# Kernel optimization log

Hardware: AMD Instinct MI355X
Metric: run time of the kernel (lower is better)

## Reference

```python
import jax, jax.numpy as jnp
import numpy as np

EPS = 1e-4
B, T = 8192, 100
SEQ = T + 1          # 101: history + appended target token
D_EMB = 36           # 2*4 + 2*4 + 2*6 + 2*4
D_MODEL = 2 * D_EMB  # 72
NUM_TASKS = 10


def pos_table(periods, freqs):
    # PositionExpansion buffer: [periods+1, 2*freqs]
    i = jnp.arange(periods + 1, dtype=jnp.float32)[:, None]
    j = jnp.arange(freqs, dtype=jnp.float32)[None, :]
    ang = (np.pi / periods) * (2.0 ** j) * (i - 1.0)
    return jnp.concatenate([jnp.sin(ang), jnp.cos(ang)], axis=1)


def robust_scale(h, eps):
    # h: [B, T] float. Vectorized version of the per-sample RobustScaler loop.
    mask = h != 0
    cnt = mask.sum(1, keepdims=True).astype(h.dtype)              # [B,1]
    safe = jnp.maximum(cnt, 1.0)
    mean = jnp.where(mask, h, 0.0).sum(1, keepdims=True) / safe
    var = jnp.where(mask, (h - mean) ** 2, 0.0).sum(1, keepdims=True) / safe
    mean = jnp.where(cnt > 0, mean, 0.0)
    std = jnp.where(cnt > 0, jnp.sqrt(var), 0.0)
    upper = mean + 2.0 * std                                      # [B,1]
    clipped = jnp.clip(h, 0.0, upper)
    mask2 = clipped != 0
    cnt2 = mask2.sum(1, keepdims=True).astype(h.dtype)
    safe2 = jnp.maximum(cnt2, 1.0)
    mc = jnp.where(mask2, clipped, 0.0).sum(1, keepdims=True) / safe2
    vc = jnp.where(mask2, (clipped - mc) ** 2, 0.0).sum(1, keepdims=True) / safe2
    mc = jnp.where(cnt2 > 0, mc, 0.0)
    sc = jnp.where(cnt2 > 0, jnp.sqrt(vc), 0.0)
    s = mc + sc + eps                                             # [B,1]
    scaled = jnp.clip(h / s, 0.0, 3.0)
    return s[:, :, None], scaled[:, :, None]                      # [B,1,1], [B,T,1]


def setup_inputs() -> dict:
    key = jax.random.key(0)
    ks = jax.random.split(key, 32)
    history = jax.random.uniform(ks[0], (B, T), jnp.float32)
    yr = jax.random.randint(ks[1], (B, T), 2000, 2011)
    mo = jax.random.randint(ks[2], (B, T), 1, 13)
    dd = jax.random.randint(ks[3], (B, T), 1, 32)
    dw = jax.random.randint(ks[4], (B, T), 0, 7)
    ts = jnp.stack([yr, mo, dd, dw], axis=-1)
    tyr = jax.random.randint(ks[5], (B,), 2000, 2011)
    tmo = jax.random.randint(ks[6], (B,), 1, 13)
    tdd = jax.random.randint(ks[7], (B,), 1, 32)
    tdw = jax.random.randint(ks[8], (B,), 0, 7)
    target_ts = jnp.stack([tyr, tmo, tdd, tdw, jnp.zeros((B,), tyr.dtype)], axis=-1)
    task = jax.random.randint(ks[9], (B,), 0, NUM_TASKS)

    def w(k, fi, fo):
        return jax.random.normal(k, (fi, fo), jnp.float32) * 0.02

    params = dict(
        w_np=w(ks[10], 1, D_EMB), b_np=jnp.zeros((D_EMB,), jnp.float32),
        w_wp=w(ks[11], 1, D_EMB), b_wp=jnp.zeros((D_EMB,), jnp.float32),
        task_emb=jax.random.normal(ks[12], (NUM_TASKS, D_EMB), jnp.float32) * 0.02,
        tw1_0=w(ks[13], SEQ, D_MODEL), tb1_0=jnp.zeros((D_MODEL,), jnp.float32),
        tw2_0=w(ks[14], D_MODEL, SEQ), tb2_0=jnp.zeros((SEQ,), jnp.float32),
        cw1_0=w(ks[15], D_MODEL, D_MODEL), cb1_0=jnp.zeros((D_MODEL,), jnp.float32),
        cw2_0=w(ks[16], D_MODEL, D_MODEL), cb2_0=jnp.zeros((D_MODEL,), jnp.float32),
        tw1_1=w(ks[17], SEQ, D_MODEL), tb1_1=jnp.zeros((D_MODEL,), jnp.float32),
        tw2_1=w(ks[18], D_MODEL, SEQ), tb2_1=jnp.zeros((SEQ,), jnp.float32),
        cw1_1=w(ks[19], D_MODEL, D_MODEL), cb1_1=jnp.zeros((D_MODEL,), jnp.float32),
        cw2_1=w(ks[20], D_MODEL, D_MODEL), cb2_1=jnp.zeros((D_MODEL,), jnp.float32),
        wp_time=w(ks[21], SEQ, 1), bp_time=jnp.zeros((1,), jnp.float32),
        w_head=w(ks[22], D_MODEL, 1), b_head=jnp.zeros((1,), jnp.float32),
    )
    return dict(history=history, ts=ts, target_ts=target_ts, task=task, **params)


def _resblock(x, tw1, tb1, tw2, tb2, cw1, cb1, cw2, cb2):
    xt = jnp.swapaxes(x, 1, 2)                                   # [B,D,SEQ]
    x = x + jnp.swapaxes(jax.nn.relu(xt @ tw1 + tb1) @ tw2 + tb2, 1, 2)
    x = x + (jax.nn.relu(x @ cw1 + cb1) @ cw2 + cb2)
    return x


def reference(history, ts, target_ts, task,
              w_np, b_np, w_wp, b_wp, task_emb,
              tw1_0, tb1_0, tw2_0, tb2_0, cw1_0, cb1_0, cw2_0, cb2_0,
              tw1_1, tb1_1, tw2_1, tb2_1, cw1_1, cb1_1, cw2_1, cb2_1,
              wp_time, bp_time, w_head, b_head):
    pe_y = pos_table(10, 4)
    pe_m = pos_table(12, 4)
    pe_d = pos_table(31, 6)
    pe_w = pos_table(7, 4)
    yr = ts[:, :, 0]
    dy = jnp.clip(yr[:, -1:] - yr, 0, 10)
    pos = jnp.concatenate([pe_y[dy], pe_m[ts[:, :, 1]], pe_d[ts[:, :, 2]], pe_w[ts[:, :, 3]]], axis=-1)  # [B,T,36]
    scale, h = robust_scale(history, EPS)                         # [B,1,1], [B,T,1]
    e0 = jax.nn.relu(h @ w_np + b_np)
    e1 = jax.nn.relu(h @ w_wp + b_wp) + pos
    hist = jnp.concatenate([e0, e1], axis=-1)                     # [B,T,72]
    tt = target_ts.reshape(-1, 1, 5)
    yrq = jnp.clip(yr[:, -1:] - tt[:, :, 0], 0, 10)
    qp = jnp.concatenate([pe_y[yrq], pe_m[tt[:, :, 1]], pe_d[tt[:, :, 2]], pe_w[tt[:, :, 3]]], axis=-1)[:, 0, :]
    t = task_emb[task]                                            # [B,36]
    tgt = jnp.concatenate([t, t + qp], axis=-1)                   # [B,72]
    x = jnp.concatenate([hist, tgt[:, None, :]], axis=1)          # [B,101,72]
    x = _resblock(x, tw1_0, tb1_0, tw2_0, tb2_0, cw1_0, cb1_0, cw2_0, cb2_0)
    x = _resblock(x, tw1_1, tb1_1, tw2_1, tb2_1, cw1_1, cb1_1, cw2_1, cb2_1)
    x = jnp.swapaxes(x, 1, 2) @ wp_time + bp_time                 # [B,72,1]
    x = jnp.swapaxes(x, 1, 2)                                     # [B,1,72]
    y = jax.nn.relu(x @ w_head + b_head)[..., 0]                  # [B,1]
    y = y * scale[:, :, 0]
    y = y + history.mean(1, keepdims=True)
    return y[:, 0], scale
```

## Files before the change

kernel.cpp:

```cpp
#include <hip/hip_runtime.h>
#include <math.h>

#define NB   8192
#define TLEN 100
#define SEQ  101
#define DE   36
#define DM   72
#define NT   512
#define NW   8
#define OPLD 104
#define OPN  10528

#define RB_SETS    71
#define TOTAL_SETS 142

typedef _Float16 half8v __attribute__((ext_vector_type(8)));
typedef __attribute__((ext_vector_type(4))) float f32x4;
union U16 { uint4 u; half8v h; };

#define MFMAH(a, b, c) __builtin_amdgcn_mfma_f32_16x16x32_f16((a), (b), (c), 0, 0, 0)

static __device__ __forceinline__ unsigned short f2h(float f) {
  union { _Float16 h; unsigned short u; } c;
  c.h = (_Float16)f;
  return c.u;
}
static __device__ __forceinline__ float h2f(unsigned short u) {
  union { _Float16 h; unsigned short u; } c;
  c.u = u;
  return (float)c.h;
}

struct SetupParams {
  const float* tw1[2]; const float* tw2[2]; const float* cw1[2]; const float* cw2[2];
  unsigned* ws;
};

__global__ void setup_kernel(SetupParams sp) {
  int s = blockIdx.x;
  int tid = threadIdx.x;
  int l = tid >> 2, r = tid & 3;
  int rb = s / RB_SETS, s2 = s % RB_SETS;
  const float* W; int K, N, ks, nt;
  if (s2 < 20)      { ks = s2 / 5;        nt = s2 % 5;        W = sp.tw1[rb]; K = SEQ; N = DM; }
  else if (s2 < 41) { int t = s2 - 20; ks = t / 7; nt = t % 7; W = sp.tw2[rb]; K = DM;  N = SEQ; }
  else if (s2 < 56) { int t = s2 - 41; ks = t / 5; nt = t % 5; W = sp.cw1[rb]; K = DM;  N = DM; }
  else              { int t = s2 - 56; ks = t / 5; nt = t % 5; W = sp.cw2[rb]; K = DM;  N = DM; }
  int g = l >> 4;
  int n = nt * 16 + (l & 15);
  int k0 = ks * 32 + g * 8 + 2 * r;
  int k1 = k0 + 1;
  float f0 = (k0 < K && n < N) ? W[k0 * N + n] : 0.f;
  float f1 = (k1 < K && n < N) ? W[k1 * N + n] : 0.f;
  union { _Float16 h; unsigned short u; } h0, h1;
  h0.h = (_Float16)f0; h1.h = (_Float16)f1;
  unsigned idx = (unsigned)s * 256u + (unsigned)l * 4u + (unsigned)r;
  sp.ws[idx] = (unsigned)h0.u | ((unsigned)h1.u << 16);
}

struct Params {
  const float *history; const int *ts; const int *target_ts; const int *task;
  const float *w_np; const float *b_np; const float *w_wp; const float *b_wp;
  const float *task_emb;
  const float *tb1[2]; const float *tb2[2]; const float *cb1[2]; const float *cb2[2];
  const float *wp_time; const float *bp_time; const float *w_head; const float *b_head;
  const uint4 *wf; float *out;
};

template<int NTN, int NTM, int KSTEPS, bool SWAP, typename Epi>
static __device__ __forceinline__ void gemm_phase_col(
    const unsigned short* __restrict__ opb,
    const uint4* __restrict__ wf, int set_base, int lane, int wave, Epi epi) {
  const int g8 = (lane >> 4) * 8;
  const int m16 = lane & 15;
  const int col    = wave % NTN;
  const int sharer = wave / NTN;
  const int nShare = (NW - 1 - col) / NTN + 1;
  uint4 wh[KSTEPS];
  #pragma unroll
  for (int ks = 0; ks < KSTEPS; ++ks) {
    size_t off = (size_t)(set_base + ks * NTN + col) * 64 + lane;
    wh[ks] = wf[off];
  }
  for (int r = sharer; r < NTM; r += nShare) {
    int mrow = r * 16 + m16; if (mrow > SEQ - 1) mrow = SEQ - 1;
    int abase = mrow * OPLD + g8;
    f32x4 a = {0.f, 0.f, 0.f, 0.f};
    #pragma unroll
    for (int ks = 0; ks < KSTEPS; ++ks) {
      half8v ah = *(const half8v*)&opb[abase + ks * 32];
      U16 h; h.u = wh[ks];
      if (SWAP) a = MFMAH(h.h, ah, a);
      else      a = MFMAH(ah, h.h, a);
    }
    epi(r, col, a);
  }
}

__global__ __launch_bounds__(NT, 4) void fpfn_kernel(Params p) {
  __shared__ __align__(16) unsigned short R1[OPN];
  __shared__ __align__(16) unsigned short R2[OPN];
  __shared__ __align__(16) unsigned short R3[OPN];
  __shared__ float pe[640];
  __shared__ float sh[TLEN];
  __shared__ unsigned short datesu[TLEN * 4];

  const int tid  = threadIdx.x;
  const int b    = blockIdx.x;
  const int lane = tid & 63;
  const int wave = tid >> 6;

  {
    uint4 z = {0, 0, 0, 0};
    uint4* z0 = (uint4*)R1;
    uint4* z1 = (uint4*)R2;
    uint4* z2 = (uint4*)R3;
    for (int i = tid; i < OPN / 8; i += NT) { z0[i] = z; z1[i] = z; z2[i] = z; }
  }

  float s = 0.f, hist_mean = 0.f;

  if (wave == 0) {
    int t1 = lane + 64;
    bool v1 = (t1 < TLEN);
    float h0 = p.history[(size_t)b * TLEN + lane];
    float h1 = v1 ? p.history[(size_t)b * TLEN + t1] : 0.f;
    auto wred = [&](float v) -> float {
      #pragma unroll
      for (int o = 32; o > 0; o >>= 1) v += __shfl_xor(v, o, 64);
      return v;
    };
    float nz0 = (h0 != 0.f) ? 1.f : 0.f;
    float nz1 = (v1 && h1 != 0.f) ? 1.f : 0.f;
    float cnt  = wred(nz0 + nz1);
    float hsum = wred(h0 + h1);
    float safe = fmaxf(cnt, 1.f);
    float mean = hsum / safe;
    float var  = wred(nz0 * (h0 - mean) * (h0 - mean) + nz1 * (h1 - mean) * (h1 - mean)) / safe;
    float mean_z = (cnt > 0.f) ? mean : 0.f;
    float std_z  = (cnt > 0.f) ? sqrtf(var) : 0.f;
    float upper  = mean_z + 2.f * std_z;
    float c0v = fminf(fmaxf(h0, 0.f), upper);
    float c1v = fminf(fmaxf(h1, 0.f), upper);
    float m0 = (c0v != 0.f) ? 1.f : 0.f;
    float m1 = (v1 && c1v != 0.f) ? 1.f : 0.f;
    float cnt2 = wred(m0 + m1);
    float csum = wred(m0 * c0v + m1 * c1v);
    float safe2 = fmaxf(cnt2, 1.f);
    float mc = csum / safe2;
    float vc = wred(m0 * (c0v - mc) * (c0v - mc) + m1 * (c1v - mc) * (c1v - mc)) / safe2;
    float mc_z = (cnt2 > 0.f) ? mc : 0.f;
    float sc_z = (cnt2 > 0.f) ? sqrtf(vc) : 0.f;
    s = mc_z + sc_z + 1e-4f;
    hist_mean = hsum * (1.f / (float)TLEN);
    sh[lane] = fminf(fmaxf(h0 / s, 0.f), 3.f);
    if (v1) sh[t1] = fminf(fmaxf(h1 / s, 0.f), 3.f);
  } else {
    for (int idx = tid - 64; idx < 640; idx += (NT - 64)) {
      int periods, freqs, row, col;
      if (idx < 88)       { periods = 10; freqs = 4; row = idx >> 3;        col = idx & 7; }
      else if (idx < 192) { periods = 12; freqs = 4; row = (idx - 88) >> 3; col = (idx - 88) & 7; }
      else if (idx < 576) { periods = 31; freqs = 6; int r2 = idx - 192; row = r2 / 12; col = r2 - row * 12; }
      else                { periods = 7;  freqs = 4; row = (idx - 576) >> 3; col = (idx - 576) & 7; }
      int jf = (col < freqs) ? col : (col - freqs);
      float pip = (float)(3.14159265358979323846 / (double)periods);
      float ang = pip * (float)(1 << jf) * ((float)row - 1.0f);
      pe[idx] = (col < freqs) ? sinf(ang) : cosf(ang);
    }
    int t = tid - 64;
    if (t < TLEN) {
      int yr99 = p.ts[((size_t)b * TLEN + (TLEN - 1)) * 4 + 0];
      const int* tsb = p.ts + ((size_t)b * TLEN + t) * 4;
      int dy = yr99 - tsb[0]; dy = dy < 0 ? 0 : (dy > 10 ? 10 : dy);
      datesu[t * 4 + 0] = (unsigned short)(dy * 8);
      datesu[t * 4 + 1] = (unsigned short)(88  + tsb[1] * 8);
      datesu[t * 4 + 2] = (unsigned short)(192 + tsb[2] * 12);
      datesu[t * 4 + 3] = (unsigned short)(576 + tsb[3] * 8);
    }
  }
  __syncthreads();

  for (int idx = tid; idx < DM * TLEN; idx += NT) {
    int j = idx / TLEN;
    int t = idx - j * TLEN;
    float sv = sh[t];
    float v;
    if (j < DE) {
      v = fmaxf(fmaf(sv, p.w_np[j], p.b_np[j]), 0.f);
    } else {
      int jj = j - DE;
      float e1 = fmaxf(fmaf(sv, p.w_wp[jj], p.b_wp[jj]), 0.f);
      float pv;
      if (jj < 8)       pv = pe[datesu[t * 4 + 0] + jj];
      else if (jj < 16) pv = pe[datesu[t * 4 + 1] + (jj - 8)];
      else if (jj < 28) pv = pe[datesu[t * 4 + 2] + (jj - 16)];
      else              pv = pe[datesu[t * 4 + 3] + (jj - 28)];
      v = e1 + pv;
    }
    unsigned short hv = f2h(v);
    R1[j * OPLD + t] = hv;
    R2[t * OPLD + j] = hv;
  }
  if (tid < DM) {
    int tk = p.task[b];
    float te = p.task_emb[tk * DE + (tid < DE ? tid : tid - DE)];
    float v = te;
    if (tid >= DE) {
      int jj = tid - DE;
      const int* tt = p.target_ts + (size_t)b * 5;
      int yr99 = p.ts[((size_t)b * TLEN + (TLEN - 1)) * 4 + 0];
      int dy = yr99 - tt[0]; dy = dy < 0 ? 0 : (dy > 10 ? 10 : dy);
      float qv;
      if (jj < 8)       qv = pe[dy * 8 + jj];
      else if (jj < 16) qv = pe[88  + tt[1] * 8  + (jj - 8)];
      else if (jj < 28) qv = pe[192 + tt[2] * 12 + (jj - 16)];
      else              qv = pe[576 + tt[3] * 8  + (jj - 28)];
      v = te + qv;
    }
    unsigned short hv = f2h(v);
    R1[tid * OPLD + (SEQ - 1)] = hv;
    R2[(SEQ - 1) * OPLD + tid] = hv;
  }
  __syncthreads();

  const int m16 = lane & 15;
  const int rowb = (lane >> 4) * 4;

  #pragma unroll 1
  for (int rb = 0; rb < 2; ++rb) {
    const int base = rb * RB_SETS;
    const float* tb1 = p.tb1[rb]; const float* tb2 = p.tb2[rb];
    const float* cb1 = p.cb1[rb]; const float* cb2 = p.cb2[rb];

    gemm_phase_col<5, 5, 4, true>(R1, p.wf, base + 0, lane, wave,
      [&](int mt, int nt, f32x4 a) {
        int c  = mt * 16 + m16;
        int j0 = nt * 16 + rowb;
        if (c < DM && j0 < DM) {
          float4 b4 = *(const float4*)&tb1[j0];
          ushort4 hx;
          hx.x = f2h(fmaxf(a[0] + b4.x, 0.f));
          hx.y = f2h(fmaxf(a[1] + b4.y, 0.f));
          hx.z = f2h(fmaxf(a[2] + b4.z, 0.f));
          hx.w = f2h(fmaxf(a[3] + b4.w, 0.f));
          *(ushort4*)&R3[c * OPLD + j0] = hx;
        }
      });
    __syncthreads();

    gemm_phase_col<7, 5, 3, false>(R3, p.wf, base + 20, lane, wave,
      [&](int mt, int nt, f32x4 a) {
        int t  = nt * 16 + m16;
        int c0 = mt * 16 + rowb;
        if (t < SEQ && c0 < DM) {
          float bias = tb2[t];
          ushort4 xo = *(const ushort4*)&R2[t * OPLD + c0];
          ushort4 hx;
          hx.x = f2h(h2f(xo.x) + a[0] + bias);
          hx.y = f2h(h2f(xo.y) + a[1] + bias);
          hx.z = f2h(h2f(xo.z) + a[2] + bias);
          hx.w = f2h(h2f(xo.w) + a[3] + bias);
          *(ushort4*)&R2[t * OPLD + c0] = hx;
        }
      });
    __syncthreads();

    gemm_phase_col<5, 7, 3, true>(R2, p.wf, base + 41, lane, wave,
      [&](int mt, int nt, f32x4 a) {
        int t  = mt * 16 + m16;
        int j0 = nt * 16 + rowb;
        if (t < SEQ && j0 < DM) {
          float4 b4 = *(const float4*)&cb1[j0];
          ushort4 hx;
          hx.x = f2h(fmaxf(a[0] + b4.x, 0.f));
          hx.y = f2h(fmaxf(a[1] + b4.y, 0.f));
          hx.z = f2h(fmaxf(a[2] + b4.z, 0.f));
          hx.w = f2h(fmaxf(a[3] + b4.w, 0.f));
          *(ushort4*)&R3[t * OPLD + j0] = hx;
        }
      });
    __syncthreads();

    gemm_phase_col<5, 7, 3, true>(R3, p.wf, base + 56, lane, wave,
      [&](int mt, int nt, f32x4 a) {
        int t  = mt * 16 + m16;
        int c0 = nt * 16 + rowb;
        if (t < SEQ && c0 < DM) {
          float4 cb4 = *(const float4*)&cb2[c0];
          ushort4 xo = *(const ushort4*)&R2[t * OPLD + c0];
          ushort4 hx;
          hx.x = f2h(h2f(xo.x) + a[0] + cb4.x);
          hx.y = f2h(h2f(xo.y) + a[1] + cb4.y);
          hx.z = f2h(h2f(xo.z) + a[2] + cb4.z);
          hx.w = f2h(h2f(xo.w) + a[3] + cb4.w);
          *(ushort4*)&R2[t * OPLD + c0] = hx;
          R1[(c0 + 0) * OPLD + t] = hx.x;
          R1[(c0 + 1) * OPLD + t] = hx.y;
          R1[(c0 + 2) * OPLD + t] = hx.z;
          R1[(c0 + 3) * OPLD + t] = hx.w;
        }
      });
    __syncthreads();
  }

  if (tid < DM) {
    float a = 0.f;
    for (int t = 0; t < SEQ; ++t) a = fmaf(h2f(R2[t * OPLD + tid]), p.wp_time[t], a);
    sh[tid] = (a + p.bp_time[0]) * p.w_head[tid];
  }
  __syncthreads();
  if (tid == 0) {
    float yv = 0.f;
    #pragma unroll 8
    for (int i = 0; i < DM; ++i) yv += sh[i];
    yv = fmaxf(yv + p.b_head[0], 0.f);
    p.out[b]      = yv * s + hist_mean;
    p.out[NB + b] = s;
  }
}

extern "C" void kernel_launch(void* const* d_in, const int* in_sizes, int n_in,
                              void* d_out, int out_size, void* d_ws, size_t ws_size,
                              hipStream_t stream) {
  (void)in_sizes; (void)n_in; (void)out_size; (void)ws_size;

  SetupParams sp;
  sp.tw1[0] = (const float*)d_in[9];  sp.tw2[0] = (const float*)d_in[11];
  sp.cw1[0] = (const float*)d_in[13]; sp.cw2[0] = (const float*)d_in[15];
  sp.tw1[1] = (const float*)d_in[17]; sp.tw2[1] = (const float*)d_in[19];
  sp.cw1[1] = (const float*)d_in[21]; sp.cw2[1] = (const float*)d_in[23];
  sp.ws = (unsigned*)d_ws;
  hipLaunchKernelGGL(setup_kernel, dim3(TOTAL_SETS), dim3(256), 0, stream, sp);

  Params p;
  p.history   = (const float*)d_in[0];
  p.ts        = (const int*)  d_in[1];
  p.target_ts = (const int*)  d_in[2];
  p.task      = (const int*)  d_in[3];
  p.w_np = (const float*)d_in[4];  p.b_np = (const float*)d_in[5];
  p.w_wp = (const float*)d_in[6];  p.b_wp = (const float*)d_in[7];
  p.task_emb = (const float*)d_in[8];
  p.tb1[0] = (const float*)d_in[10]; p.tb2[0] = (const float*)d_in[12];
  p.cb1[0] = (const float*)d_in[14]; p.cb2[0] = (const float*)d_in[16];
  p.tb1[1] = (const float*)d_in[18]; p.tb2[1] = (const float*)d_in[20];
  p.cb1[1] = (const float*)d_in[22]; p.cb2[1] = (const float*)d_in[24];
  p.wp_time = (const float*)d_in[25]; p.bp_time = (const float*)d_in[26];
  p.w_head  = (const float*)d_in[27]; p.b_head  = (const float*)d_in[28];
  p.wf  = (const uint4*)d_ws;
  p.out = (float*)d_out;
  hipLaunchKernelGGL(fpfn_kernel, dim3(NB), dim3(NT), 0, stream, p);
}
```

Before: 337.3 us.

## Prefetch next phase weights into registers and pair MFMA row tiles

Splits the per-phase GEMM into a weight-load step and a compute step, so each phase's weight fragments are fetched from global memory while the previous phase computes. The first weights are loaded before the initial barrier. The compute loop also handles two row tiles per iteration with independent accumulators, which exposes more MFMA-level parallelism. The cost is higher register pressure from the extra weight buffers and second accumulator, which could limit occupancy under the 4-blocks launch bound.

```diff
diff --git a/kernel.cpp b/kernel.cpp
--- a/kernel.cpp
+++ b/kernel.cpp
@@ -67,33 +67,46 @@
   const uint4 *wf; float *out;
 };
 
+template<int NTN, int KSTEPS>
+static __device__ __forceinline__ void load_w(
+    const uint4* __restrict__ wf, int set_base, int lane, int wave, uint4* wh) {
+  const int col = wave % NTN;
+  #pragma unroll
+  for (int ks = 0; ks < KSTEPS; ++ks)
+    wh[ks] = wf[(size_t)(set_base + ks * NTN + col) * 64 + lane];
+}
+
 template<int NTN, int NTM, int KSTEPS, bool SWAP, typename Epi>
-static __device__ __forceinline__ void gemm_phase_col(
-    const unsigned short* __restrict__ opb,
-    const uint4* __restrict__ wf, int set_base, int lane, int wave, Epi epi) {
+static __device__ __forceinline__ void compute_phase(
+    const unsigned short* __restrict__ opb, const uint4* wh,
+    int lane, int wave, Epi epi) {
   const int g8 = (lane >> 4) * 8;
   const int m16 = lane & 15;
   const int col    = wave % NTN;
   const int sharer = wave / NTN;
   const int nShare = (NW - 1 - col) / NTN + 1;
-  uint4 wh[KSTEPS];
-  #pragma unroll
-  for (int ks = 0; ks < KSTEPS; ++ks) {
-    size_t off = (size_t)(set_base + ks * NTN + col) * 64 + lane;
-    wh[ks] = wf[off];
-  }
-  for (int r = sharer; r < NTM; r += nShare) {
-    int mrow = r * 16 + m16; if (mrow > SEQ - 1) mrow = SEQ - 1;
-    int abase = mrow * OPLD + g8;
-    f32x4 a = {0.f, 0.f, 0.f, 0.f};
+  int r = sharer;
+  while (r < NTM) {
+    int r2 = r + nShare;
+    bool has2 = r2 < NTM;
+    int r2c = has2 ? r2 : r;
+    int mrow1 = r * 16 + m16;   if (mrow1 > SEQ - 1) mrow1 = SEQ - 1;
+    int mrow2 = r2c * 16 + m16; if (mrow2 > SEQ - 1) mrow2 = SEQ - 1;
+    int ab1 = mrow1 * OPLD + g8;
+    int ab2 = mrow2 * OPLD + g8;
+    f32x4 a1 = {0.f, 0.f, 0.f, 0.f};
+    f32x4 a2 = {0.f, 0.f, 0.f, 0.f};
     #pragma unroll
     for (int ks = 0; ks < KSTEPS; ++ks) {
-      half8v ah = *(const half8v*)&opb[abase + ks * 32];
+      half8v ah1 = *(const half8v*)&opb[ab1 + ks * 32];
+      half8v ah2 = *(const half8v*)&opb[ab2 + ks * 32];
       U16 h; h.u = wh[ks];
-      if (SWAP) a = MFMAH(h.h, ah, a);
-      else      a = MFMAH(ah, h.h, a);
-    }
-    epi(r, col, a);
+      if (SWAP) { a1 = MFMAH(h.h, ah1, a1); a2 = MFMAH(h.h, ah2, a2); }
+      else      { a1 = MFMAH(ah1, h.h, a1); a2 = MFMAH(ah2, h.h, a2); }
+    }
+    epi(r, col, a1);
+    if (has2) epi(r2, col, a2);
+    r = r2 + nShare;
   }
 }
 
@@ -221,10 +234,13 @@
     R1[tid * OPLD + (SEQ - 1)] = hv;
     R2[(SEQ - 1) * OPLD + tid] = hv;
   }
-  __syncthreads();
 
   const int m16 = lane & 15;
   const int rowb = (lane >> 4) * 4;
+
+  uint4 whA[4], whB[3], whC[3], whD[3];
+  load_w<5, 4>(p.wf, 0, lane, wave, whA);
+  __syncthreads();
 
   #pragma unroll 1
   for (int rb = 0; rb < 2; ++rb) {
@@ -232,7 +248,8 @@
     const float* tb1 = p.tb1[rb]; const float* tb2 = p.tb2[rb];
     const float* cb1 = p.cb1[rb]; const float* cb2 = p.cb2[rb];
 
-    gemm_phase_col<5, 5, 4, true>(R1, p.wf, base + 0, lane, wave,
+    load_w<7, 3>(p.wf, base + 20, lane, wave, whB);
+    compute_phase<5, 5, 4, true>(R1, whA, lane, wave,
       [&](int mt, int nt, f32x4 a) {
         int c  = mt * 16 + m16;
         int j0 = nt * 16 + rowb;
@@ -248,7 +265,8 @@
       });
     __syncthreads();
 
-    gemm_phase_col<7, 5, 3, false>(R3, p.wf, base + 20, lane, wave,
+    load_w<5, 3>(p.wf, base + 41, lane, wave, whC);
+    compute_phase<7, 5, 3, false>(R3, whB, lane, wave,
       [&](int mt, int nt, f32x4 a) {
         int t  = nt * 16 + m16;
         int c0 = mt * 16 + rowb;
@@ -265,7 +283,8 @@
       });
     __syncthreads();
 
-    gemm_phase_col<5, 7, 3, true>(R2, p.wf, base + 41, lane, wave,
+    load_w<5, 3>(p.wf, base + 56, lane, wave, whD);
+    compute_phase<5, 7, 3, true>(R2, whC, lane, wave,
       [&](int mt, int nt, f32x4 a) {
         int t  = mt * 16 + m16;
         int j0 = nt * 16 + rowb;
@@ -281,7 +300,8 @@
       });
     __syncthreads();
 
-    gemm_phase_col<5, 7, 3, true>(R3, p.wf, base + 56, lane, wave,
+    if (rb == 0) load_w<5, 4>(p.wf, RB_SETS + 0, lane, wave, whA);
+    compute_phase<5, 7, 3, true>(R3, whD, lane, wave,
       [&](int mt, int nt, f32x4 a) {
         int t  = mt * 16 + m16;
         int c0 = nt * 16 + rowb;
```

After: 346.7 us. +2.8%, slower.

## Assign 2-column tile blocks per wave to reuse A-fragment loads across MFMAs

Applied to the files above, without the earlier changes.

Replaces the one-column-per-wave GEMM split with a hand-tuned per-wave assignment of row ranges and up to two column tiles. Each A fragment read from LDS is reused for two MFMA output tiles, cutting LDS reads, and the work is spread more evenly across the 8 waves. It costs twice the weight registers per wave, which could lower occupancy at 4 blocks per CU, and the hand-written partition tables must cover every tile exactly.

```diff
diff --git a/kernel.cpp b/kernel.cpp
--- a/kernel.cpp
+++ b/kernel.cpp
@@ -67,33 +67,43 @@
   const uint4 *wf; float *out;
 };
 
-template<int NTN, int NTM, int KSTEPS, bool SWAP, typename Epi>
-static __device__ __forceinline__ void gemm_phase_col(
+template<int NTN, int KSTEPS, bool SWAP, typename Epi>
+static __device__ __forceinline__ void gemm_phase_nb(
     const unsigned short* __restrict__ opb,
-    const uint4* __restrict__ wf, int set_base, int lane, int wave, Epi epi) {
+    const uint4* __restrict__ wf, int set_base, int lane,
+    int r0, int nr, int c0, int nc, Epi epi) {
   const int g8 = (lane >> 4) * 8;
   const int m16 = lane & 15;
-  const int col    = wave % NTN;
-  const int sharer = wave / NTN;
-  const int nShare = (NW - 1 - col) / NTN + 1;
-  uint4 wh[KSTEPS];
+  const int c1 = (nc > 1) ? c0 + 1 : c0;
+  uint4 w0[KSTEPS], w1[KSTEPS];
   #pragma unroll
   for (int ks = 0; ks < KSTEPS; ++ks) {
-    size_t off = (size_t)(set_base + ks * NTN + col) * 64 + lane;
-    wh[ks] = wf[off];
-  }
-  for (int r = sharer; r < NTM; r += nShare) {
+    w0[ks] = wf[(size_t)(set_base + ks * NTN + c0) * 64 + lane];
+    w1[ks] = wf[(size_t)(set_base + ks * NTN + c1) * 64 + lane];
+  }
+  for (int i = 0; i < nr; ++i) {
+    int r = r0 + i;
     int mrow = r * 16 + m16; if (mrow > SEQ - 1) mrow = SEQ - 1;
-    int abase = mrow * OPLD + g8;
-    f32x4 a = {0.f, 0.f, 0.f, 0.f};
+    int ab = mrow * OPLD + g8;
+    half8v ah[KSTEPS];
+    #pragma unroll
+    for (int ks = 0; ks < KSTEPS; ++ks) ah[ks] = *(const half8v*)&opb[ab + ks * 32];
+    f32x4 a0 = {0.f, 0.f, 0.f, 0.f};
     #pragma unroll
     for (int ks = 0; ks < KSTEPS; ++ks) {
-      half8v ah = *(const half8v*)&opb[abase + ks * 32];
-      U16 h; h.u = wh[ks];
-      if (SWAP) a = MFMAH(h.h, ah, a);
-      else      a = MFMAH(ah, h.h, a);
-    }
-    epi(r, col, a);
+      U16 h; h.u = w0[ks];
+      a0 = SWAP ? MFMAH(h.h, ah[ks], a0) : MFMAH(ah[ks], h.h, a0);
+    }
+    epi(r, c0, a0);
+    if (nc > 1) {
+      f32x4 a1 = {0.f, 0.f, 0.f, 0.f};
+      #pragma unroll
+      for (int ks = 0; ks < KSTEPS; ++ks) {
+        U16 h; h.u = w1[ks];
+        a1 = SWAP ? MFMAH(h.h, ah[ks], a1) : MFMAH(ah[ks], h.h, a1);
+      }
+      epi(r, c0 + 1, a1);
+    }
   }
 }
 
@@ -226,13 +236,22 @@
   const int m16 = lane & 15;
   const int rowb = (lane >> 4) * 4;
 
+  int Ar0, Anr, Ac0, Anc;
+  if (wave < 6) { Ac0 = (wave / 3) * 2; Anc = 2; int sub = wave % 3; Ar0 = sub * 2; Anr = (sub < 2) ? 2 : 1; }
+  else          { Ac0 = 4; Anc = 1; int sub = wave - 6; Ar0 = sub * 3; Anr = sub ? 2 : 3; }
+  int Br0, Bnr, Bc0, Bnc;
+  { int pr = wave >> 1; Bc0 = pr * 2; Bnc = (pr < 3) ? 2 : 1; int sub = wave & 1; Br0 = sub * 3; Bnr = sub ? 2 : 3; }
+  int Cr0, Cnr, Cc0, Cnc;
+  if (wave < 6) { Cc0 = (wave / 3) * 2; Cnc = 2; int sub = wave % 3; Cr0 = sub * 2; Cnr = (sub < 2) ? 2 : 3; }
+  else          { Cc0 = 4; Cnc = 1; int sub = wave - 6; Cr0 = sub * 4; Cnr = sub ? 3 : 4; }
+
   #pragma unroll 1
   for (int rb = 0; rb < 2; ++rb) {
     const int base = rb * RB_SETS;
     const float* tb1 = p.tb1[rb]; const float* tb2 = p.tb2[rb];
     const float* cb1 = p.cb1[rb]; const float* cb2 = p.cb2[rb];
 
-    gemm_phase_col<5, 5, 4, true>(R1, p.wf, base + 0, lane, wave,
+    gemm_phase_nb<5, 4, true>(R1, p.wf, base + 0, lane, Ar0, Anr, Ac0, Anc,
       [&](int mt, int nt, f32x4 a) {
         int c  = mt * 16 + m16;
         int j0 = nt * 16 + rowb;
@@ -248,7 +267,7 @@
       });
     __syncthreads();
 
-    gemm_phase_col<7, 5, 3, false>(R3, p.wf, base + 20, lane, wave,
+    gemm_phase_nb<7, 3, false>(R3, p.wf, base + 20, lane, Br0, Bnr, Bc0, Bnc,
       [&](int mt, int nt, f32x4 a) {
         int t  = nt * 16 + m16;
         int c0 = mt * 16 + rowb;
@@ -265,7 +284,7 @@
       });
     __syncthreads();
 
-    gemm_phase_col<5, 7, 3, true>(R2, p.wf, base + 41, lane, wave,
+    gemm_phase_nb<5, 3, true>(R2, p.wf, base + 41, lane, Cr0, Cnr, Cc0, Cnc,
       [&](int mt, int nt, f32x4 a) {
         int t  = mt * 16 + m16;
         int j0 = nt * 16 + rowb;
@@ -281,7 +300,7 @@
       });
     __syncthreads();
 
-    gemm_phase_col<5, 7, 3, true>(R3, p.wf, base + 56, lane, wave,
+    gemm_phase_nb<5, 3, true>(R3, p.wf, base + 56, lane, Cr0, Cnr, Cc0, Cnc,
       [&](int mt, int nt, f32x4 a) {
         int t  = mt * 16 + m16;
         int c0 = nt * 16 + rowb;
```

Result: no change. 337.5 us, median of 2 (+0.0%).
